# Performance work log

Measured on AMD Instinct MI355X. Metric: run time of the kernel, lower is better.

## Reference

```python
import jax, jax.numpy as jnp
import numpy as np

L, B, D = 1024, 32, 1024
USE_TANH = True  # use_tanh=1

def setup_inputs() -> dict:
    key = jax.random.key(0)
    k1, k2, k3, k4 = jax.random.split(key, 4)
    return {
        "x": jax.random.normal(k1, (L, B, D), jnp.float32),
        "c0": jax.random.normal(k2, (B, D), jnp.float32),
        "weight": jax.random.normal(k3, (D, D, 3), jnp.float32) * 0.02,
        "bias": jax.random.normal(k4, (2 * D,), jnp.float32) * 0.02,
    }

def reference(x, c0, weight, bias):
    # x: [L,B,D], weight: [D_in, D_out, 3], bias: [2*D_out], c0: [B,D_out]
    d = weight.shape[1]
    # u = x @ weight.view(n_in, 3*n_out) with per-output-dim interleaving -> [L,B,D,3]
    u = jnp.einsum('lbi,iok->lbok', x, weight)
    u0 = u[..., 0]                       # candidate
    f = jax.nn.sigmoid(u[..., 1] + bias[:d])    # forget gate
    r = jax.nn.sigmoid(u[..., 2] + bias[d:])    # highway/reset gate

    def step(c_prev, inp):
        f_t, u0_t = inp
        c_t = f_t * c_prev + (1.0 - f_t) * u0_t
        return c_t, c_t

    _, c = jax.lax.scan(step, c0, (f, u0))  # c: [L,B,D]
    g = jnp.tanh(c) if USE_TANH else c
    h = r * g + (1.0 - r) * x               # highway connection (n_in == n_out path)
    return h, c
```

## Files before the change

kernel.cpp:

```cpp
#include <hip/hip_runtime.h>
#include <hip/hip_bf16.h>
#include <stdint.h>

#define L_DIM 1024
#define B_DIM 32
#define D_DIM 1024
#define M_DIM (L_DIM * B_DIM)
#define N3_DIM (3 * D_DIM)
#define K_DIM D_DIM
#define LBD ((int64_t)L_DIM * B_DIM * D_DIM)
#define NBD (B_DIM * D_DIM)
#define NCHUNK 32
#define CLEN 32

#define BM 128
#define BN 128
#define BK 64
#define NMT (M_DIM / BM)
#define NNT (N3_DIM / BN)
#define NKT (K_DIM / BK)

typedef __bf16 bf16_t;
typedef bf16_t bf16x8 __attribute__((ext_vector_type(8)));
typedef float f32x4 __attribute__((ext_vector_type(4)));

__device__ __forceinline__ unsigned short f2bf(float f) {
    union { float f; unsigned u; } v; v.f = f;
    unsigned u = v.u;
    u += 0x7FFFu + ((u >> 16) & 1u);
    return (unsigned short)(u >> 16);
}
__device__ __forceinline__ float bf2f(unsigned short h) {
    union { unsigned u; float f; } v; v.u = ((unsigned)h) << 16;
    return v.f;
}

__global__ void cvt_x_kernel(const float* __restrict__ x, unsigned short* __restrict__ xb) {
    int64_t i0 = ((int64_t)blockIdx.x * blockDim.x + threadIdx.x) * 4;
    int64_t stride = (int64_t)gridDim.x * blockDim.x * 4;
    for (int64_t i = i0; i < LBD; i += stride) {
        float4 v = *reinterpret_cast<const float4*>(x + i);
        ushort4 o;
        o.x = f2bf(v.x); o.y = f2bf(v.y); o.z = f2bf(v.z); o.w = f2bf(v.w);
        *reinterpret_cast<ushort4*>(xb + i) = o;
    }
}

__global__ void cvt_w_kernel(const float* __restrict__ w, unsigned short* __restrict__ wT) {
    __shared__ float tile[64][65];
    int bid = blockIdx.x;
    int k  = bid >> 8;
    int o0 = ((bid >> 4) & 15) * 64;
    int i0 = (bid & 15) * 64;
    int t = threadIdx.x;
    {
        int o = t & 63, ib = t >> 6;
        #pragma unroll
        for (int it = 0; it < 16; ++it) {
            int i = ib + it * 4;
            tile[o][i] = w[((int64_t)(i0 + i) * 1024 + (o0 + o)) * 3 + k];
        }
    }
    __syncthreads();
    {
        int i = t & 63, ob = t >> 6;
        #pragma unroll
        for (int ot = 0; ot < 16; ++ot) {
            int o = ob + ot * 4;
            wT[(int64_t)(k * 1024 + o0 + o) * 1024 + (i0 + i)] = f2bf(tile[o][i]);
        }
    }
}

__device__ __forceinline__ void gload_lds16(const void* g, void* l) {
    __builtin_amdgcn_global_load_lds(
        (const __attribute__((address_space(1))) unsigned int*)g,
        (__attribute__((address_space(3))) unsigned int*)l,
        16, 0, 0);
}

__global__ __launch_bounds__(256, 2) void gemm_kernel(
    const unsigned short* __restrict__ A,
    const unsigned short* __restrict__ Bt,
    const float* __restrict__ bias,
    float* __restrict__ u0_out,
    unsigned short* __restrict__ fb,
    unsigned short* __restrict__ rb)
{
    __shared__ __align__(16) unsigned short a_tile[128 * 64];
    __shared__ __align__(16) unsigned short b_tile[128 * 64];

    int bid = blockIdx.x;
    int xcd = bid & 7, local = bid >> 3;
    int nt = xcd * 3 + (local % 3);
    int mt = local / 3;
    int m0 = mt * BM, n0 = nt * BN;

    int tid = threadIdx.x;
    int w = tid >> 6, lane = tid & 63;
    int wr = (w >> 1) * 64, wc = (w & 1) * 64;
    int l15 = lane & 15, l4 = lane >> 4;
    int pcx = l15 & 7;

    int sr = lane >> 3;
    int sc = ((lane & 7) ^ sr) << 3;
    const unsigned short* Abase = A  + (int64_t)(m0 + sr) * K_DIM + sc;
    const unsigned short* Bbase = Bt + (int64_t)(n0 + sr) * K_DIM + sc;

    f32x4 acc[4][4];
    #pragma unroll
    for (int i = 0; i < 4; ++i)
        #pragma unroll
        for (int j = 0; j < 4; ++j) acc[i][j] = (f32x4){0.f, 0.f, 0.f, 0.f};

    for (int kt = 0; kt < NKT; ++kt) {
        int k0 = kt * BK;
        __syncthreads();
        #pragma unroll
        for (int i = 0; i < 4; ++i) {
            int r0 = (i * 4 + w) * 8;
            gload_lds16(Abase + (int64_t)r0 * K_DIM + k0, &a_tile[r0 * 64]);
            gload_lds16(Bbase + (int64_t)r0 * K_DIM + k0, &b_tile[r0 * 64]);
        }
        __syncthreads();

        #pragma unroll
        for (int ks = 0; ks < 2; ++ks) {
            int pc = ((ks * 4 + l4) ^ pcx) << 3;
            bf16x8 af[4], bf[4];
            #pragma unroll
            for (int im = 0; im < 4; ++im)
                af[im] = *reinterpret_cast<const bf16x8*>(&a_tile[(wr + im * 16 + l15) * 64 + pc]);
            #pragma unroll
            for (int jn = 0; jn < 4; ++jn)
                bf[jn] = *reinterpret_cast<const bf16x8*>(&b_tile[(wc + jn * 16 + l15) * 64 + pc]);
            #pragma unroll
            for (int im = 0; im < 4; ++im)
                #pragma unroll
                for (int jn = 0; jn < 4; ++jn)
                    acc[im][jn] = __builtin_amdgcn_mfma_f32_16x16x32_bf16(
                        af[im], bf[jn], acc[im][jn], 0, 0, 0);
        }
    }

    int region = n0 >> 10;
    #pragma unroll
    for (int im = 0; im < 4; ++im) {
        #pragma unroll
        for (int jn = 0; jn < 4; ++jn) {
            f32x4 v = acc[im][jn];
            int row0 = m0 + wr + im * 16 + l4 * 4;
            int col  = (n0 + wc + jn * 16 + l15) & 1023;
            #pragma unroll
            for (int jj = 0; jj < 4; ++jj) {
                int64_t idx = (int64_t)(row0 + jj) * 1024 + col;
                float val = v[jj];
                if (region == 0) {
                    u0_out[idx] = val;
                } else if (region == 1) {
                    fb[idx] = f2bf(1.0f / (1.0f + __expf(-(val + bias[col]))));
                } else {
                    rb[idx] = f2bf(1.0f / (1.0f + __expf(-(val + bias[1024 + col]))));
                }
            }
        }
    }
}


__global__ void scan_phase1(const unsigned short* __restrict__ fb,
                            const float* __restrict__ u0_arr,
                            float* __restrict__ Aout, float* __restrict__ Bout) {
    int t = blockIdx.x * blockDim.x + threadIdx.x;
    int idx = t & (NBD - 1);
    int chunk = t >> 15;
    int64_t base = (int64_t)chunk * CLEN * NBD + idx;
    float Ap = 1.0f, Bv = 0.0f;
    #pragma unroll 8
    for (int i = 0; i < CLEN; ++i, base += NBD) {
        float f = bf2f(fb[base]);
        float u0 = u0_arr[base];
        Bv = u0 + f * (Bv - u0);
        Ap *= f;
    }
    Aout[t] = Ap; Bout[t] = Bv;
}

__global__ void scan_phase2(const float* __restrict__ c0, const float* __restrict__ Aarr,
                            const float* __restrict__ Barr, float* __restrict__ cin) {
    int idx = blockIdx.x * blockDim.x + threadIdx.x;
    float c = c0[idx];
    #pragma unroll
    for (int ch = 0; ch < NCHUNK; ++ch) {
        cin[ch * NBD + idx] = c;
        c = Aarr[ch * NBD + idx] * c + Barr[ch * NBD + idx];
    }
}

__global__ void scan_phase3(const float* __restrict__ x,
                            const unsigned short* __restrict__ fb,
                            const unsigned short* __restrict__ rb,
                            const float* __restrict__ cin,
                            float* __restrict__ out_h, float* __restrict__ out_c) {
    int t = blockIdx.x * blockDim.x + threadIdx.x;
    int idx = t & (NBD - 1);
    int chunk = t >> 15;
    float c = cin[t];
    int64_t base = (int64_t)chunk * CLEN * NBD + idx;
    #pragma unroll 4
    for (int i = 0; i < CLEN; ++i, base += NBD) {
        float f  = bf2f(fb[base]);
        float u0 = out_c[base];
        c = u0 + f * (c - u0);
        out_c[base] = c;
        float e = __expf(2.0f * c);
        float g = (e - 1.0f) / (e + 1.0f);
        float r = bf2f(rb[base]);
        float xv = x[base];
        out_h[base] = xv + r * (g - xv);
    }
}

extern "C" void kernel_launch(void* const* d_in, const int* in_sizes, int n_in,
                              void* d_out, int out_size, void* d_ws, size_t ws_size,
                              hipStream_t stream) {
    const float* x    = (const float*)d_in[0];
    const float* c0   = (const float*)d_in[1];
    const float* wgt  = (const float*)d_in[2];
    const float* bias = (const float*)d_in[3];
    float* out = (float*)d_out;

    unsigned short* xb = (unsigned short*)d_ws;
    unsigned short* wT = xb + (int64_t)M_DIM * K_DIM;
    unsigned short* fb = wT + (int64_t)N3_DIM * K_DIM;
    unsigned short* rb = fb + LBD;

    float* Aarr = (float*)d_ws;
    float* Barr = Aarr + NCHUNK * NBD;
    float* cin  = Barr + NCHUNK * NBD;

    cvt_x_kernel<<<8192, 256, 0, stream>>>(x, xb);
    cvt_w_kernel<<<768, 256, 0, stream>>>(wgt, wT);
    gemm_kernel<<<NMT * NNT, 256, 0, stream>>>(xb, wT, bias, out + LBD, fb, rb);
    scan_phase1<<<(NCHUNK * NBD) / 256, 256, 0, stream>>>(fb, out + LBD, Aarr, Barr);
    scan_phase2<<<NBD / 256, 256, 0, stream>>>(c0, Aarr, Barr, cin);
    scan_phase3<<<(NCHUNK * NBD) / 256, 256, 0, stream>>>(x, fb, rb, cin, out, out + LBD);
}
```

Baseline: 506.0 us.

## Merge conversion kernels, store u0 as bf16, raise GEMM occupancy bound

Merges the x and weight conversion kernels into one launch, with block ranges choosing the path. When the workspace is large enough, the GEMM writes the candidate u0 as bf16 to a workspace buffer instead of fp32 into the c output, and the scan phases read that buffer. This halves u0 traffic but adds bf16 rounding to the recurrence input. The GEMM launch bound rises from 2 to 4 blocks per CU, which may force register spills.

```diff
diff --git a/kernel.cpp b/kernel.cpp
--- a/kernel.cpp
+++ b/kernel.cpp
@@ -35,39 +35,41 @@
     return v.f;
 }
 
-__global__ void cvt_x_kernel(const float* __restrict__ x, unsigned short* __restrict__ xb) {
-    int64_t i0 = ((int64_t)blockIdx.x * blockDim.x + threadIdx.x) * 4;
-    int64_t stride = (int64_t)gridDim.x * blockDim.x * 4;
-    for (int64_t i = i0; i < LBD; i += stride) {
-        float4 v = *reinterpret_cast<const float4*>(x + i);
-        ushort4 o;
-        o.x = f2bf(v.x); o.y = f2bf(v.y); o.z = f2bf(v.z); o.w = f2bf(v.w);
-        *reinterpret_cast<ushort4*>(xb + i) = o;
-    }
-}
-
-__global__ void cvt_w_kernel(const float* __restrict__ w, unsigned short* __restrict__ wT) {
+__global__ void cvt_kernel(const float* __restrict__ x, unsigned short* __restrict__ xb,
+                           const float* __restrict__ w, unsigned short* __restrict__ wT) {
     __shared__ float tile[64][65];
     int bid = blockIdx.x;
-    int k  = bid >> 8;
-    int o0 = ((bid >> 4) & 15) * 64;
-    int i0 = (bid & 15) * 64;
-    int t = threadIdx.x;
-    {
-        int o = t & 63, ib = t >> 6;
-        #pragma unroll
-        for (int it = 0; it < 16; ++it) {
-            int i = ib + it * 4;
-            tile[o][i] = w[((int64_t)(i0 + i) * 1024 + (o0 + o)) * 3 + k];
-        }
-    }
-    __syncthreads();
-    {
-        int i = t & 63, ob = t >> 6;
-        #pragma unroll
-        for (int ot = 0; ot < 16; ++ot) {
-            int o = ob + ot * 4;
-            wT[(int64_t)(k * 1024 + o0 + o) * 1024 + (i0 + i)] = f2bf(tile[o][i]);
+    if (bid < 8192) {
+        int64_t i0 = ((int64_t)bid * blockDim.x + threadIdx.x) * 4;
+        const int64_t stride = (int64_t)8192 * 256 * 4;
+        for (int64_t i = i0; i < LBD; i += stride) {
+            float4 v = *reinterpret_cast<const float4*>(x + i);
+            ushort4 o;
+            o.x = f2bf(v.x); o.y = f2bf(v.y); o.z = f2bf(v.z); o.w = f2bf(v.w);
+            *reinterpret_cast<ushort4*>(xb + i) = o;
+        }
+    } else {
+        int wb = bid - 8192;
+        int k  = wb >> 8;
+        int o0 = ((wb >> 4) & 15) * 64;
+        int i0 = (wb & 15) * 64;
+        int t = threadIdx.x;
+        {
+            int o = t & 63, ib = t >> 6;
+            #pragma unroll
+            for (int it = 0; it < 16; ++it) {
+                int i = ib + it * 4;
+                tile[o][i] = w[((int64_t)(i0 + i) * 1024 + (o0 + o)) * 3 + k];
+            }
+        }
+        __syncthreads();
+        {
+            int i = t & 63, ob = t >> 6;
+            #pragma unroll
+            for (int ot = 0; ot < 16; ++ot) {
+                int o = ob + ot * 4;
+                wT[(int64_t)(k * 1024 + o0 + o) * 1024 + (i0 + i)] = f2bf(tile[o][i]);
+            }
         }
     }
 }
@@ -79,13 +81,15 @@
         16, 0, 0);
 }
 
-__global__ __launch_bounds__(256, 2) void gemm_kernel(
+__global__ __launch_bounds__(256, 4) void gemm_kernel(
     const unsigned short* __restrict__ A,
     const unsigned short* __restrict__ Bt,
     const float* __restrict__ bias,
     float* __restrict__ u0_out,
     unsigned short* __restrict__ fb,
-    unsigned short* __restrict__ rb)
+    unsigned short* __restrict__ rb,
+    unsigned short* __restrict__ u0b,
+    int useU0b)
 {
     __shared__ __align__(16) unsigned short a_tile[128 * 64];
     __shared__ __align__(16) unsigned short b_tile[128 * 64];
@@ -156,7 +160,8 @@
                 int64_t idx = (int64_t)(row0 + jj) * 1024 + col;
                 float val = v[jj];
                 if (region == 0) {
-                    u0_out[idx] = val;
+                    if (useU0b) u0b[idx] = f2bf(val);
+                    else        u0_out[idx] = val;
                 } else if (region == 1) {
                     fb[idx] = f2bf(1.0f / (1.0f + __expf(-(val + bias[col]))));
                 } else {
@@ -169,19 +174,30 @@
 
 
 __global__ void scan_phase1(const unsigned short* __restrict__ fb,
-                            const float* __restrict__ u0_arr,
+                            const float* __restrict__ u0f,
+                            const unsigned short* __restrict__ u0b, int useU0b,
                             float* __restrict__ Aout, float* __restrict__ Bout) {
     int t = blockIdx.x * blockDim.x + threadIdx.x;
     int idx = t & (NBD - 1);
     int chunk = t >> 15;
     int64_t base = (int64_t)chunk * CLEN * NBD + idx;
     float Ap = 1.0f, Bv = 0.0f;
-    #pragma unroll 8
-    for (int i = 0; i < CLEN; ++i, base += NBD) {
-        float f = bf2f(fb[base]);
-        float u0 = u0_arr[base];
-        Bv = u0 + f * (Bv - u0);
-        Ap *= f;
+    if (useU0b) {
+        #pragma unroll 8
+        for (int i = 0; i < CLEN; ++i, base += NBD) {
+            float f = bf2f(fb[base]);
+            float u0 = bf2f(u0b[base]);
+            Bv = u0 + f * (Bv - u0);
+            Ap *= f;
+        }
+    } else {
+        #pragma unroll 8
+        for (int i = 0; i < CLEN; ++i, base += NBD) {
+            float f = bf2f(fb[base]);
+            float u0 = u0f[base];
+            Bv = u0 + f * (Bv - u0);
+            Ap *= f;
+        }
     }
     Aout[t] = Ap; Bout[t] = Bv;
 }
@@ -200,6 +216,7 @@
 __global__ void scan_phase3(const float* __restrict__ x,
                             const unsigned short* __restrict__ fb,
                             const unsigned short* __restrict__ rb,
+                            const unsigned short* __restrict__ u0b, int useU0b,
                             const float* __restrict__ cin,
                             float* __restrict__ out_h, float* __restrict__ out_c) {
     int t = blockIdx.x * blockDim.x + threadIdx.x;
@@ -207,17 +224,32 @@
     int chunk = t >> 15;
     float c = cin[t];
     int64_t base = (int64_t)chunk * CLEN * NBD + idx;
-    #pragma unroll 4
-    for (int i = 0; i < CLEN; ++i, base += NBD) {
-        float f  = bf2f(fb[base]);
-        float u0 = out_c[base];
-        c = u0 + f * (c - u0);
-        out_c[base] = c;
-        float e = __expf(2.0f * c);
-        float g = (e - 1.0f) / (e + 1.0f);
-        float r = bf2f(rb[base]);
-        float xv = x[base];
-        out_h[base] = xv + r * (g - xv);
+    if (useU0b) {
+        #pragma unroll 4
+        for (int i = 0; i < CLEN; ++i, base += NBD) {
+            float f  = bf2f(fb[base]);
+            float u0 = bf2f(u0b[base]);
+            c = u0 + f * (c - u0);
+            out_c[base] = c;
+            float e = __expf(2.0f * c);
+            float g = (e - 1.0f) / (e + 1.0f);
+            float r = bf2f(rb[base]);
+            float xv = x[base];
+            out_h[base] = xv + r * (g - xv);
+        }
+    } else {
+        #pragma unroll 4
+        for (int i = 0; i < CLEN; ++i, base += NBD) {
+            float f  = bf2f(fb[base]);
+            float u0 = out_c[base];
+            c = u0 + f * (c - u0);
+            out_c[base] = c;
+            float e = __expf(2.0f * c);
+            float g = (e - 1.0f) / (e + 1.0f);
+            float r = bf2f(rb[base]);
+            float xv = x[base];
+            out_h[base] = xv + r * (g - xv);
+        }
     }
 }
 
@@ -234,15 +266,17 @@
     unsigned short* wT = xb + (int64_t)M_DIM * K_DIM;
     unsigned short* fb = wT + (int64_t)N3_DIM * K_DIM;
     unsigned short* rb = fb + LBD;
+    size_t need = ((size_t)M_DIM * K_DIM + (size_t)N3_DIM * K_DIM + 3 * (size_t)LBD) * 2;
+    int useU0b = (ws_size >= need) ? 1 : 0;
+    unsigned short* u0b = useU0b ? (rb + LBD) : nullptr;
 
     float* Aarr = (float*)d_ws;
     float* Barr = Aarr + NCHUNK * NBD;
     float* cin  = Barr + NCHUNK * NBD;
 
-    cvt_x_kernel<<<8192, 256, 0, stream>>>(x, xb);
-    cvt_w_kernel<<<768, 256, 0, stream>>>(wgt, wT);
-    gemm_kernel<<<NMT * NNT, 256, 0, stream>>>(xb, wT, bias, out + LBD, fb, rb);
-    scan_phase1<<<(NCHUNK * NBD) / 256, 256, 0, stream>>>(fb, out + LBD, Aarr, Barr);
+    cvt_kernel<<<8960, 256, 0, stream>>>(x, xb, wgt, wT);
+    gemm_kernel<<<NMT * NNT, 256, 0, stream>>>(xb, wT, bias, out + LBD, fb, rb, u0b, useU0b);
+    scan_phase1<<<(NCHUNK * NBD) / 256, 256, 0, stream>>>(fb, out + LBD, u0b, useU0b, Aarr, Barr);
     scan_phase2<<<NBD / 256, 256, 0, stream>>>(c0, Aarr, Barr, cin);
-    scan_phase3<<<(NCHUNK * NBD) / 256, 256, 0, stream>>>(x, fb, rb, cin, out, out + LBD);
-}
+    scan_phase3<<<(NCHUNK * NBD) / 256, 256, 0, stream>>>(x, fb, rb, u0b, useU0b, cin, out, out + LBD);
+}
```

Result: faster. 465.8 us (-8.0%).
